# Kernel optimization log

Measured on AMD Instinct MI355X. Metric: run time of the kernel, lower is better.

The kernel has to match this reference:

```python
import jax, jax.numpy as jnp
import numpy as np

N_NODES = 20000
NEG_SLOPE = 0.01  # F.leaky_relu default


def _gcn_norm(edge_index, edge_weight, n):
    # PyG GCNConv(normalize=True, improved=True): add self-loops with weight 2.0,
    # then symmetric normalization deg^{-1/2} * w * deg^{-1/2}.
    row, col = edge_index[0], edge_index[1]
    loop = jnp.arange(n, dtype=edge_index.dtype)
    row = jnp.concatenate([row, loop])
    col = jnp.concatenate([col, loop])
    w = jnp.concatenate([edge_weight, jnp.full((n,), 2.0, edge_weight.dtype)])
    deg = jax.ops.segment_sum(w, col, num_segments=n)
    dinv = jnp.where(deg > 0, jax.lax.rsqrt(deg), 0.0)
    norm = dinv[row] * w * dinv[col]
    return row, col, norm


def setup_inputs() -> dict:
    key = jax.random.key(0)
    ks = jax.random.split(key, 6)
    F, N, D, O, E = 3, N_NODES, 256, 256, 320000
    x = jax.random.normal(ks[0], (F, N, D), jnp.float32)
    edge_index = jax.random.randint(ks[1], (2, E), 0, N, jnp.int32)
    edge_weight = jax.random.uniform(ks[2], (E,), jnp.float32)
    s = (1.0 / np.sqrt(D)).astype(np.float32) if hasattr(np.sqrt(D), 'astype') else 1.0 / np.sqrt(D)
    Wg = jax.random.uniform(ks[3], (F, D, O), jnp.float32, -s, s)   # GCNConv weight per field
    Wr = jax.random.uniform(ks[4], (F, O, D), jnp.float32, -s, s)   # nn.Linear weight [out,in]
    Wh = jax.random.uniform(ks[5], (F, D, O), jnp.float32, -s, s)   # HighWay gate weight
    return {"x": x, "edge_index": edge_index, "edge_weight": edge_weight,
            "Wg": Wg, "Wr": Wr, "Wh": Wh}


def reference(x, edge_index, edge_weight, Wg, Wr, Wh):
    n = x.shape[1]
    row, col, norm = _gcn_norm(edge_index, edge_weight, n)
    # GCNConv: transform then propagate (sum over incoming normalized edges)
    xg = jnp.einsum('fnd,fdo->fno', x, Wg)            # [F,N,O]
    msg = xg[:, row, :] * norm[None, :, None]          # [F,E+N,O]
    gcn_rep = jax.vmap(lambda m: jax.ops.segment_sum(m, col, num_segments=n))(msg)
    # residual linear (nn.Linear, no bias): x @ Wr^T
    res_rep = jnp.einsum('fnd,fod->fno', x, Wr)
    # highway gate: sigmoid(x @ Wh); out = gate*gcn + (1-gate)*res
    gate = jax.nn.sigmoid(jnp.einsum('fnd,fdo->fno', x, Wh))
    rep = gate * gcn_rep + (1.0 - gate) * res_rep
    return jnp.where(rep >= 0, rep, NEG_SLOPE * rep)   # leaky_relu
```

## Files before the change

### kernel.cpp

```cpp
#include <hip/hip_runtime.h>
#include <math.h>

#define NFIELD 3
#define FEAT 256
#define CAP  64

typedef __attribute__((ext_vector_type(8))) short frag_ab;
typedef __attribute__((ext_vector_type(4))) float frag_cd;

__device__ __forceinline__ unsigned short f2bf(float f) {
    unsigned int u = __float_as_uint(f);
    u = (u + 0x7fffu + ((u >> 16) & 1u)) >> 16;
    return (unsigned short)u;
}
__device__ __forceinline__ float bf2f(unsigned short b) {
    return __uint_as_float(((unsigned int)b) << 16);
}

__device__ __forceinline__ void gld16(const unsigned short* g, unsigned short* l) {
    __builtin_amdgcn_global_load_lds(
        (const __attribute__((address_space(1))) void*)g,
        (__attribute__((address_space(3))) void*)l, 16, 0, 0);
}

__global__ __launch_bounds__(256) void k_prep0(
        float* __restrict__ deg, int* __restrict__ cnt, int n,
        const float* __restrict__ Wg, const float* __restrict__ Wr,
        const float* __restrict__ Wh,
        unsigned short* __restrict__ wgT, unsigned short* __restrict__ wrT,
        unsigned short* __restrict__ whT,
        const float* __restrict__ x, unsigned short* __restrict__ xb, int nfld) {
    int gtid = blockIdx.x * 256 + threadIdx.x;
    int gsz  = gridDim.x * 256;

    for (int i = gtid; i < n; i += gsz) { deg[i] = 2.0f; cnt[i] = 0; }

    for (int i = gtid; i < NFIELD * FEAT * FEAT; i += gsz) {
        int f = i >> 16;
        int r = i & 0xffff;
        int d = r >> 8;
        int o = r & 255;
        int tdst = (f << 16) | (o << 8) | d;
        wgT[tdst] = f2bf(Wg[i]);
        whT[tdst] = f2bf(Wh[i]);
        wrT[i]    = f2bf(Wr[i]);
    }

    int nq = n * (FEAT / 4);
    int cnt4 = nfld * nq;
    for (int i = gtid; i < cnt4; i += gsz) {
        int f = i / nq;
        int r = i - f * nq;
        int node = r >> 6;
        int q = r & 63;
        float4 v = *((const float4*)x + i);
        ushort4 o;
        o.x = f2bf(v.x); o.y = f2bf(v.y); o.z = f2bf(v.z); o.w = f2bf(v.w);
        ((ushort4*)xb)[((size_t)node * nfld + f) * 64 + q] = o;
    }
}

__global__ void k_scatter(const int* __restrict__ ei, const float* __restrict__ ew,
                          float* __restrict__ deg, int* __restrict__ cnt,
                          int2* __restrict__ bucket, int E) {
    int e = blockIdx.x * blockDim.x + threadIdx.x;
    if (e < E) {
        int r = ei[e];
        int c = ei[E + e];
        float w = ew[e];
        atomicAdd(&deg[c], w);
        int slot = atomicAdd(&cnt[c], 1);
        if (slot < CAP)
            bucket[(size_t)c * CAP + slot] = make_int2(r, __float_as_int(w));
    }
}

__global__ void k_gather(const int2* __restrict__ bucket,
                         const float* __restrict__ deg, const int* __restrict__ cnt,
                         const unsigned short* __restrict__ xb,
                         unsigned short* __restrict__ xab,
                         int n, int fl_count) {
    int wid  = blockIdx.x * (blockDim.x >> 6) + (threadIdx.x >> 6);
    int lane = threadIdx.x & 63;
    if (wid >= n) return;
    int c = wid;
    int beg = c * CAP;
    int end = beg + min(cnt[c], CAP);
    float dc = rsqrtf(deg[c]);
    float s  = 2.0f * dc * dc;
    const size_t stride = (size_t)fl_count * FEAT;

    float acc[NFIELD][4];
    const unsigned short* pc = xb + (size_t)c * stride;
    #pragma unroll
    for (int fl = 0; fl < NFIELD; ++fl) {
        if (fl >= fl_count) break;
        ushort4 v = ((const ushort4*)(pc + fl * FEAT))[lane];
        acc[fl][0] = s * bf2f(v.x); acc[fl][1] = s * bf2f(v.y);
        acc[fl][2] = s * bf2f(v.z); acc[fl][3] = s * bf2f(v.w);
    }

    int i = beg;
    if (fl_count == NFIELD) {
        for (; i + 3 < end; i += 4) {
            int4 qa = *(const int4*)&bucket[i];
            int4 qb = *(const int4*)&bucket[i + 2];
            float d0 = deg[qa.x];
            float d1 = deg[qa.z];
            float d2 = deg[qb.x];
            float d3 = deg[qb.z];
            const unsigned short* p0 = xb + (size_t)qa.x * (NFIELD * FEAT);
            const unsigned short* p1 = xb + (size_t)qa.z * (NFIELD * FEAT);
            const unsigned short* p2 = xb + (size_t)qb.x * (NFIELD * FEAT);
            const unsigned short* p3 = xb + (size_t)qb.z * (NFIELD * FEAT);
            float n0 = rsqrtf(d0) * __int_as_float(qa.y) * dc;
            float n1 = rsqrtf(d1) * __int_as_float(qa.w) * dc;
            float n2 = rsqrtf(d2) * __int_as_float(qb.y) * dc;
            float n3 = rsqrtf(d3) * __int_as_float(qb.w) * dc;
            ushort4 v[4][NFIELD];
            v[0][0] = ((const ushort4*)p0)[lane];
            v[1][0] = ((const ushort4*)p1)[lane];
            v[2][0] = ((const ushort4*)p2)[lane];
            v[3][0] = ((const ushort4*)p3)[lane];
            v[0][1] = ((const ushort4*)(p0 + FEAT))[lane];
            v[1][1] = ((const ushort4*)(p1 + FEAT))[lane];
            v[2][1] = ((const ushort4*)(p2 + FEAT))[lane];
            v[3][1] = ((const ushort4*)(p3 + FEAT))[lane];
            v[0][2] = ((const ushort4*)(p0 + 2 * FEAT))[lane];
            v[1][2] = ((const ushort4*)(p1 + 2 * FEAT))[lane];
            v[2][2] = ((const ushort4*)(p2 + 2 * FEAT))[lane];
            v[3][2] = ((const ushort4*)(p3 + 2 * FEAT))[lane];
            #pragma unroll
            for (int fl = 0; fl < NFIELD; ++fl) {
                acc[fl][0] += n0 * bf2f(v[0][fl].x) + n1 * bf2f(v[1][fl].x)
                            + n2 * bf2f(v[2][fl].x) + n3 * bf2f(v[3][fl].x);
                acc[fl][1] += n0 * bf2f(v[0][fl].y) + n1 * bf2f(v[1][fl].y)
                            + n2 * bf2f(v[2][fl].y) + n3 * bf2f(v[3][fl].y);
                acc[fl][2] += n0 * bf2f(v[0][fl].z) + n1 * bf2f(v[1][fl].z)
                            + n2 * bf2f(v[2][fl].z) + n3 * bf2f(v[3][fl].z);
                acc[fl][3] += n0 * bf2f(v[0][fl].w) + n1 * bf2f(v[1][fl].w)
                            + n2 * bf2f(v[2][fl].w) + n3 * bf2f(v[3][fl].w);
            }
        }
        for (; i + 1 < end; i += 2) {
            int4 qa = *(const int4*)&bucket[i];
            float d0 = deg[qa.x];
            float d1 = deg[qa.z];
            const unsigned short* pa = xb + (size_t)qa.x * (NFIELD * FEAT);
            const unsigned short* pb = xb + (size_t)qa.z * (NFIELD * FEAT);
            float na = rsqrtf(d0) * __int_as_float(qa.y) * dc;
            float nb = rsqrtf(d1) * __int_as_float(qa.w) * dc;
            ushort4 va0 = ((const ushort4*)pa)[lane];
            ushort4 vb0 = ((const ushort4*)pb)[lane];
            ushort4 va1 = ((const ushort4*)(pa + FEAT))[lane];
            ushort4 vb1 = ((const ushort4*)(pb + FEAT))[lane];
            ushort4 va2 = ((const ushort4*)(pa + 2 * FEAT))[lane];
            ushort4 vb2 = ((const ushort4*)(pb + 2 * FEAT))[lane];
            acc[0][0] += na * bf2f(va0.x) + nb * bf2f(vb0.x);
            acc[0][1] += na * bf2f(va0.y) + nb * bf2f(vb0.y);
            acc[0][2] += na * bf2f(va0.z) + nb * bf2f(vb0.z);
            acc[0][3] += na * bf2f(va0.w) + nb * bf2f(vb0.w);
            acc[1][0] += na * bf2f(va1.x) + nb * bf2f(vb1.x);
            acc[1][1] += na * bf2f(va1.y) + nb * bf2f(vb1.y);
            acc[1][2] += na * bf2f(va1.z) + nb * bf2f(vb1.z);
            acc[1][3] += na * bf2f(va1.w) + nb * bf2f(vb1.w);
            acc[2][0] += na * bf2f(va2.x) + nb * bf2f(vb2.x);
            acc[2][1] += na * bf2f(va2.y) + nb * bf2f(vb2.y);
            acc[2][2] += na * bf2f(va2.z) + nb * bf2f(vb2.z);
            acc[2][3] += na * bf2f(va2.w) + nb * bf2f(vb2.w);
        }
        for (; i < end; ++i) {
            int2 ra = bucket[i];
            float d0 = deg[ra.x];
            const unsigned short* pa = xb + (size_t)ra.x * (NFIELD * FEAT);
            float na = rsqrtf(d0) * __int_as_float(ra.y) * dc;
            ushort4 va0 = ((const ushort4*)pa)[lane];
            ushort4 va1 = ((const ushort4*)(pa + FEAT))[lane];
            ushort4 va2 = ((const ushort4*)(pa + 2 * FEAT))[lane];
            acc[0][0] += na * bf2f(va0.x); acc[0][1] += na * bf2f(va0.y);
            acc[0][2] += na * bf2f(va0.z); acc[0][3] += na * bf2f(va0.w);
            acc[1][0] += na * bf2f(va1.x); acc[1][1] += na * bf2f(va1.y);
            acc[1][2] += na * bf2f(va1.z); acc[1][3] += na * bf2f(va1.w);
            acc[2][0] += na * bf2f(va2.x); acc[2][1] += na * bf2f(va2.y);
            acc[2][2] += na * bf2f(va2.z); acc[2][3] += na * bf2f(va2.w);
        }
    } else {
        for (; i < end; ++i) {
            int2 ra = bucket[i];
            float d0 = deg[ra.x];
            const unsigned short* pa = xb + (size_t)ra.x * FEAT;
            float na = rsqrtf(d0) * __int_as_float(ra.y) * dc;
            ushort4 va0 = ((const ushort4*)pa)[lane];
            acc[0][0] += na * bf2f(va0.x); acc[0][1] += na * bf2f(va0.y);
            acc[0][2] += na * bf2f(va0.z); acc[0][3] += na * bf2f(va0.w);
        }
    }

    unsigned short* po = xab + (size_t)c * stride;
    #pragma unroll
    for (int fl = 0; fl < NFIELD; ++fl) {
        if (fl >= fl_count) break;
        ushort4 o;
        o.x = f2bf(acc[fl][0]); o.y = f2bf(acc[fl][1]);
        o.z = f2bf(acc[fl][2]); o.w = f2bf(acc[fl][3]);
        ((ushort4*)(po + fl * FEAT))[lane] = o;
    }
}

#define BM 64
#define BN 128
#define BK 32

__device__ __forceinline__ int swz(int row, int quad) {
    return (quad ^ ((row >> 1) & 3)) * 8;
}

__global__ __launch_bounds__(256) void k_gemm_mfma(
    const unsigned short* __restrict__ xb, const unsigned short* __restrict__ xab,
    const unsigned short* __restrict__ wgT, const unsigned short* __restrict__ wrT,
    const unsigned short* __restrict__ whT,
    float* __restrict__ out, int n, int f_base, int nfld) {

    __shared__ unsigned short As_x[BM][BK];
    __shared__ unsigned short As_a[BM][BK];
    __shared__ unsigned short Bs[3][BN][BK];

    int fl = blockIdx.z;
    int f  = f_base + fl;
    int m0 = blockIdx.x * BM;
    int o0 = blockIdx.y * BN;
    int t  = threadIdx.x;

    const unsigned short* wsrc0 = wgT + ((size_t)f << 16);
    const unsigned short* wsrc1 = wrT + ((size_t)f << 16);
    const unsigned short* wsrc2 = whT + ((size_t)f << 16);

    int w    = t >> 6;
    int lane = t & 63;
    int lrow = lane & 15;
    int quad = lane >> 4;
    int wn   = w * 32;

    frag_cd acc[3][4][2];
    #pragma unroll
    for (int s = 0; s < 3; ++s)
        #pragma unroll
        for (int mi = 0; mi < 4; ++mi)
            #pragma unroll
            for (int ni = 0; ni < 2; ++ni)
                acc[s][mi][ni] = (frag_cd){0.f, 0.f, 0.f, 0.f};

    int a_row  = 16 * w + (lane >> 2);
    int a_csrc = ((lane & 3) ^ ((a_row >> 1) & 3)) * 8;
    int am     = min(m0 + a_row, n - 1);
    const unsigned short* a_src_x = xb  + ((size_t)am * nfld + fl) * FEAT + a_csrc;
    const unsigned short* a_src_a = xab + ((size_t)am * nfld + fl) * FEAT + a_csrc;
    unsigned short* a_dst_x = &As_x[16 * w][0];
    unsigned short* a_dst_a = &As_a[16 * w][0];

    const unsigned short* b_src[6];
    unsigned short*       b_dst[6];
    #pragma unroll
    for (int j = 0; j < 6; ++j) {
        int si  = 6 * w + j;
        int buf = si >> 3;
        int row = (si & 7) * 16 + (lane >> 2);
        int cs  = ((lane & 3) ^ ((row >> 1) & 3)) * 8;
        const unsigned short* ws = (buf == 0) ? wsrc0 : (buf == 1) ? wsrc1 : wsrc2;
        b_src[j] = ws + ((size_t)(o0 + row) << 8) + cs;
        b_dst[j] = &Bs[buf][(si & 7) * 16][0];
    }

    for (int k0 = 0; k0 < FEAT; k0 += BK) {
        gld16(a_src_x, a_dst_x);
        gld16(a_src_a, a_dst_a);
        #pragma unroll
        for (int j = 0; j < 6; ++j)
            gld16(b_src[j], b_dst[j]);
        a_src_x += BK; a_src_a += BK;
        #pragma unroll
        for (int j = 0; j < 6; ++j) b_src[j] += BK;
        __syncthreads();

        frag_ab ax[4], aa[4], bg[2], br[2], bh[2];
        #pragma unroll
        for (int mi = 0; mi < 4; ++mi) {
            int r = mi * 16 + lrow;
            int c = swz(r, quad);
            ax[mi] = *(const frag_ab*)&As_x[r][c];
            aa[mi] = *(const frag_ab*)&As_a[r][c];
        }
        #pragma unroll
        for (int ni = 0; ni < 2; ++ni) {
            int r = wn + ni * 16 + lrow;
            int c = swz(r, quad);
            bg[ni] = *(const frag_ab*)&Bs[0][r][c];
            br[ni] = *(const frag_ab*)&Bs[1][r][c];
            bh[ni] = *(const frag_ab*)&Bs[2][r][c];
        }
        #pragma unroll
        for (int mi = 0; mi < 4; ++mi)
            #pragma unroll
            for (int ni = 0; ni < 2; ++ni) {
                acc[0][mi][ni] = __builtin_amdgcn_mfma_f32_16x16x32_bf16(aa[mi], bg[ni], acc[0][mi][ni], 0, 0, 0);
                acc[1][mi][ni] = __builtin_amdgcn_mfma_f32_16x16x32_bf16(ax[mi], br[ni], acc[1][mi][ni], 0, 0, 0);
                acc[2][mi][ni] = __builtin_amdgcn_mfma_f32_16x16x32_bf16(ax[mi], bh[ni], acc[2][mi][ni], 0, 0, 0);
            }
        __syncthreads();
    }

    #pragma unroll
    for (int mi = 0; mi < 4; ++mi)
        #pragma unroll
        for (int ni = 0; ni < 2; ++ni)
            #pragma unroll
            for (int i = 0; i < 4; ++i) {
                int grow = m0 + mi * 16 + quad * 4 + i;
                if (grow >= n) continue;
                float h = acc[2][mi][ni][i];
                float g = 1.0f / (1.0f + __expf(-h));
                float v = g * acc[0][mi][ni][i] + (1.0f - g) * acc[1][mi][ni][i];
                v = v >= 0.0f ? v : 0.01f * v;
                out[((size_t)f * n + grow) * FEAT + o0 + wn + ni * 16 + lrow] = v;
            }
}


static inline size_t align_up(size_t v, size_t a) { return (v + a - 1) & ~(a - 1); }

extern "C" void kernel_launch(void* const* d_in, const int* in_sizes, int n_in,
                              void* d_out, int out_size, void* d_ws, size_t ws_size,
                              hipStream_t stream) {
    const float* x  = (const float*)d_in[0];
    const int*   ei = (const int*)d_in[1];
    const float* ew = (const float*)d_in[2];
    const float* Wg = (const float*)d_in[3];
    const float* Wr = (const float*)d_in[4];
    const float* Wh = (const float*)d_in[5];
    float* out = (float*)d_out;

    const int n = in_sizes[0] / (NFIELD * FEAT);
    const int E = in_sizes[2];

    char* base = (char*)d_ws;
    size_t off = 0;
    float* deg    = (float*)(base + off); off = align_up(off + (size_t)n * 4, 256);
    int*   cnt    = (int*)  (base + off); off = align_up(off + (size_t)n * 4, 256);
    int2*  bucket = (int2*) (base + off); off = align_up(off + (size_t)n * CAP * 8, 256);
    unsigned short* wgT = (unsigned short*)(base + off); off = align_up(off + (size_t)NFIELD * FEAT * FEAT * 2, 256);
    unsigned short* wrT = (unsigned short*)(base + off); off = align_up(off + (size_t)NFIELD * FEAT * FEAT * 2, 256);
    unsigned short* whT = (unsigned short*)(base + off); off = align_up(off + (size_t)NFIELD * FEAT * FEAT * 2, 256);
    size_t fixed = off;

    const size_t per_field = (size_t)n * FEAT * 2;
    int fl;
    if (ws_size >= fixed + 2 * (size_t)NFIELD * per_field + 1024) fl = NFIELD;
    else fl = 1;
    unsigned short* xb  = (unsigned short*)(base + fixed);
    unsigned short* xab = (unsigned short*)(base + align_up(fixed + (size_t)fl * per_field, 256));

    int gblocks = (n + 3) / 4;
    dim3 ggemm((n + BM - 1) / BM, FEAT / BN, fl);

    if (fl == NFIELD) {
        k_prep0  <<<2048, 256, 0, stream>>>(deg, cnt, n, Wg, Wr, Wh,
                                            wgT, wrT, whT, x, xb, NFIELD);
        k_scatter<<<(E + 255) / 256, 256, 0, stream>>>(ei, ew, deg, cnt, bucket, E);
        k_gather <<<gblocks, 256, 0, stream>>>(bucket, deg, cnt, xb, xab, n, NFIELD);
        k_gemm_mfma<<<ggemm, 256, 0, stream>>>(xb, xab, wgT, wrT, whT, out, n, 0, NFIELD);
    } else {
        for (int f = 0; f < NFIELD; ++f) {
            k_prep0  <<<2048, 256, 0, stream>>>(deg, cnt, n, Wg, Wr, Wh,
                                                wgT, wrT, whT,
                                                x + (size_t)f * n * FEAT, xb, 1);
            k_scatter<<<(E + 255) / 256, 256, 0, stream>>>(ei, ew, deg, cnt, bucket, E);
            k_gather <<<gblocks, 256, 0, stream>>>(bucket, deg, cnt, xb, xab, n, 1);
            k_gemm_mfma<<<ggemm, 256, 0, stream>>>(xb, xab, wgT, wrT, whT, out, n, f, 1);
        }
    }
}
```

Before: 283.0 us.

## Double-buffer LDS tiles in fused MFMA GEMM to overlap loads with compute

The fused three-GEMM MFMA kernel now keeps two copies of its A and B shared-memory tiles. The next K-slice is loaded directly into LDS while MFMAs run on the current one, so each step needs one barrier instead of two. The aim is to hide global-to-LDS load latency behind compute, at the cost of twice the LDS footprint (about 40KB per block), which may lower occupancy. The __syncthreads after the first STAGE may not wait for the asynchronous LDS-direct loads unless the compiler inserts a vmcnt wait, which is a correctness risk.

```diff
diff --git a/kernel.cpp b/kernel.cpp
--- a/kernel.cpp
+++ b/kernel.cpp
@@ -210,6 +210,7 @@
 #define BM 64
 #define BN 128
 #define BK 32
+#define NT (FEAT / BK)
 
 __device__ __forceinline__ int swz(int row, int quad) {
     return (quad ^ ((row >> 1) & 3)) * 8;
@@ -221,9 +222,9 @@
     const unsigned short* __restrict__ whT,
     float* __restrict__ out, int n, int f_base, int nfld) {
 
-    __shared__ unsigned short As_x[BM][BK];
-    __shared__ unsigned short As_a[BM][BK];
-    __shared__ unsigned short Bs[3][BN][BK];
+    __shared__ unsigned short As_x[2][BM][BK];
+    __shared__ unsigned short As_a[2][BM][BK];
+    __shared__ unsigned short Bs[2][3][BN][BK];
 
     int fl = blockIdx.z;
     int f  = f_base + fl;
@@ -255,48 +256,44 @@
     int am     = min(m0 + a_row, n - 1);
     const unsigned short* a_src_x = xb  + ((size_t)am * nfld + fl) * FEAT + a_csrc;
     const unsigned short* a_src_a = xab + ((size_t)am * nfld + fl) * FEAT + a_csrc;
-    unsigned short* a_dst_x = &As_x[16 * w][0];
-    unsigned short* a_dst_a = &As_a[16 * w][0];
 
     const unsigned short* b_src[6];
-    unsigned short*       b_dst[6];
+    int b_buf3[6], b_row0[6];
     #pragma unroll
     for (int j = 0; j < 6; ++j) {
         int si  = 6 * w + j;
-        int buf = si >> 3;
-        int row = (si & 7) * 16 + (lane >> 2);
+        b_buf3[j] = si >> 3;
+        b_row0[j] = (si & 7) * 16;
+        int row = b_row0[j] + (lane >> 2);
         int cs  = ((lane & 3) ^ ((row >> 1) & 3)) * 8;
-        const unsigned short* ws = (buf == 0) ? wsrc0 : (buf == 1) ? wsrc1 : wsrc2;
+        const unsigned short* ws = (b_buf3[j] == 0) ? wsrc0 : (b_buf3[j] == 1) ? wsrc1 : wsrc2;
         b_src[j] = ws + ((size_t)(o0 + row) << 8) + cs;
-        b_dst[j] = &Bs[buf][(si & 7) * 16][0];
-    }
-
-    for (int k0 = 0; k0 < FEAT; k0 += BK) {
-        gld16(a_src_x, a_dst_x);
-        gld16(a_src_a, a_dst_a);
+    }
+
+    auto STAGE = [&](int b, int koff) {
+        gld16(a_src_x + koff, &As_x[b][16 * w][0]);
+        gld16(a_src_a + koff, &As_a[b][16 * w][0]);
         #pragma unroll
         for (int j = 0; j < 6; ++j)
-            gld16(b_src[j], b_dst[j]);
-        a_src_x += BK; a_src_a += BK;
-        #pragma unroll
-        for (int j = 0; j < 6; ++j) b_src[j] += BK;
-        __syncthreads();
-
+            gld16(b_src[j] + koff, &Bs[b][b_buf3[j]][b_row0[j]][0]);
+    };
+
+    auto COMPUTE = [&](int b) {
         frag_ab ax[4], aa[4], bg[2], br[2], bh[2];
         #pragma unroll
         for (int mi = 0; mi < 4; ++mi) {
             int r = mi * 16 + lrow;
             int c = swz(r, quad);
-            ax[mi] = *(const frag_ab*)&As_x[r][c];
-            aa[mi] = *(const frag_ab*)&As_a[r][c];
+            ax[mi] = *(const frag_ab*)&As_x[b][r][c];
+            aa[mi] = *(const frag_ab*)&As_a[b][r][c];
         }
         #pragma unroll
         for (int ni = 0; ni < 2; ++ni) {
             int r = wn + ni * 16 + lrow;
             int c = swz(r, quad);
-            bg[ni] = *(const frag_ab*)&Bs[0][r][c];
-            br[ni] = *(const frag_ab*)&Bs[1][r][c];
-            bh[ni] = *(const frag_ab*)&Bs[2][r][c];
+            bg[ni] = *(const frag_ab*)&Bs[b][0][r][c];
+            br[ni] = *(const frag_ab*)&Bs[b][1][r][c];
+            bh[ni] = *(const frag_ab*)&Bs[b][2][r][c];
         }
         #pragma unroll
         for (int mi = 0; mi < 4; ++mi)
@@ -306,8 +303,18 @@
                 acc[1][mi][ni] = __builtin_amdgcn_mfma_f32_16x16x32_bf16(ax[mi], br[ni], acc[1][mi][ni], 0, 0, 0);
                 acc[2][mi][ni] = __builtin_amdgcn_mfma_f32_16x16x32_bf16(ax[mi], bh[ni], acc[2][mi][ni], 0, 0, 0);
             }
+    };
+
+    STAGE(0, 0);
+    __syncthreads();
+
+    #pragma unroll
+    for (int tt = 0; tt < NT - 1; ++tt) {
+        STAGE((tt & 1) ^ 1, (tt + 1) * BK);
+        COMPUTE(tt & 1);
         __syncthreads();
     }
+    COMPUTE((NT - 1) & 1);
 
     #pragma unroll
     for (int mi = 0; mi < 4; ++mi)
```

After: 282.3 us, median of 2. About the same (-0.2%).
